# Optimization experiments

Hardware: AMD Instinct MI355X
Metric: run time of the kernel (lower is better)

## Reference

```python
import jax, jax.numpy as jnp
import numpy as np

# Dimensions (Llama-3-8B-style GQA with paged KV cache)
B, S, HID = 1, 1024, 4096
H, HKV, D = 32, 8, 128
G = H // HKV
BLK = 16            # tokens per KV block
NB = 256            # blocks in storage
CB = 192            # context blocks attended (3072 tokens)
PAST = 2048         # tokens already cached before this step
NL = 2              # layers in kv_ptr
L = CB * BLK


def rotate_half(x):
    x1, x2 = x[..., : x.shape[-1] // 2], x[..., x.shape[-1] // 2:]
    return jnp.concatenate([-x2, x1], axis=-1)


def setup_inputs() -> dict:
    key = jax.random.key(0)
    ks = jax.random.split(key, 8)
    hidden_states = jax.random.normal(ks[0], (B, S, HID), jnp.float32)
    kv_ptr = jax.random.normal(ks[1], (NL, 2, NB, HKV, BLK, D), jnp.float32)
    Wq = 0.02 * jax.random.normal(ks[2], (H * D, HID), jnp.float32)
    Wk = 0.02 * jax.random.normal(ks[3], (HKV * D, HID), jnp.float32)
    Wv = 0.02 * jax.random.normal(ks[4], (HKV * D, HID), jnp.float32)
    Wo = 0.02 * jax.random.normal(ks[5], (HID, H * D), jnp.float32)
    # RoPE cache for the new tokens (global positions PAST..PAST+S-1), HF convention
    pos = (PAST + jnp.arange(S)).astype(jnp.float32)
    inv_freq = 1.0 / (10000.0 ** (jnp.arange(0, D, 2, dtype=jnp.float32) / D))
    freqs = pos[:, None] * inv_freq[None, :]                # [S, D/2]
    emb = jnp.concatenate([freqs, freqs], axis=-1)           # [S, D]
    cos = jnp.cos(emb)[None, None]                           # [1,1,S,D]
    sin = jnp.sin(emb)[None, None]
    new_q_lut = jnp.arange(S, dtype=jnp.int32)[None]         # identity query LUT
    new_kv_lut = (CB - S // BLK + jnp.arange(S // BLK, dtype=jnp.int32))[None]  # blocks 128..191
    all_kv_lut = jnp.arange(CB, dtype=jnp.int32)[None]       # blocks 0..191
    kv_pos = jnp.arange(L)
    q_pos = PAST + jnp.arange(S)
    mask = (kv_pos[None, None, :] <= q_pos[None, :, None])   # [1,S,L] causal over global positions
    cmd_groups = jnp.zeros((B, S), jnp.int32)                # split-K scheduling metadata (no math effect)
    return dict(hidden_states=hidden_states, kv_ptr=kv_ptr, new_q_lut=new_q_lut,
                new_kv_lut=new_kv_lut, all_kv_lut=all_kv_lut, mask=mask,
                cmd_groups=cmd_groups, cos=cos, sin=sin, Wq=Wq, Wk=Wk, Wv=Wv, Wo=Wo,
                layer_idx=0)


def reference(hidden_states, kv_ptr, new_q_lut, new_kv_lut, all_kv_lut, mask,
              cmd_groups, cos, sin, Wq, Wk, Wv, Wo, layer_idx):
    b, s, _ = hidden_states.shape
    # QKV projections (no bias)
    q = jnp.einsum('bsh,oh->bso', hidden_states, Wq).reshape(b, s, H, D).transpose(0, 2, 1, 3)
    k = jnp.einsum('bsh,oh->bso', hidden_states, Wk).reshape(b, s, HKV, D).transpose(0, 2, 1, 3)
    v = jnp.einsum('bsh,oh->bso', hidden_states, Wv).reshape(b, s, HKV, D).transpose(0, 2, 1, 3)
    # RoPE
    q = q * cos + rotate_half(q) * sin
    k = k * cos + rotate_half(k) * sin
    # fill_kv_block_storage: scatter new K/V blocks into this layer's storage (b == 1)
    kb = jnp.transpose(k[0].reshape(HKV, s // BLK, BLK, D), (1, 0, 2, 3))  # [nblk,HKV,BLK,D]
    vb = jnp.transpose(v[0].reshape(HKV, s // BLK, BLK, D), (1, 0, 2, 3))
    sk = kv_ptr[layer_idx, 0].at[new_kv_lut[0]].set(kb)
    sv = kv_ptr[layer_idx, 1].at[new_kv_lut[0]].set(vb)
    # qkv_attention: gather context blocks via LUT, masked GQA attention
    ck = jnp.transpose(sk[all_kv_lut[0]], (1, 0, 2, 3)).reshape(HKV, L, D)  # [HKV,L,D]
    cv = jnp.transpose(sv[all_kv_lut[0]], (1, 0, 2, 3)).reshape(HKV, L, D)
    qg = q[:, :, new_q_lut[0], :].reshape(b, HKV, G, s, D)
    scores = jnp.einsum('bkgsd,kld->bkgsl', qg, ck) / jnp.sqrt(jnp.float32(D))
    scores = jnp.where(mask[:, None, None], scores, jnp.finfo(scores.dtype).min)
    p = jax.nn.softmax(scores, axis=-1)
    o = jnp.einsum('bkgsl,kld->bkgsd', p, cv).reshape(b, H, s, D)
    o = o.transpose(0, 2, 1, 3).reshape(b, s, H * D)
    return jnp.einsum('bso,ho->bsh', o, Wo)
```

## Files before the change

kernel.cpp:

```cpp
#include <hip/hip_runtime.h>
#include <cstdint>
#include <cstddef>


typedef _Float16 f16;
typedef f16 f16x8 __attribute__((ext_vector_type(8)));
typedef f16 f16x4 __attribute__((ext_vector_type(4)));
typedef float f32x4 __attribute__((ext_vector_type(4)));

#define HIDN 4096
#define LCTX 3072
#define PASTN 2048
#define QK_SCALE_LOG2 0.12753102734366334f
#define RESC_THR 11.54f

__device__ __forceinline__ f32x4 mfma16(f16x8 a, f16x8 b, f32x4 c) {
    return __builtin_amdgcn_mfma_f32_16x16x32_f16(a, b, c, 0, 0, 0);
}

__device__ __forceinline__ void gl_lds16(const void* g, void* l) {
    auto gp = (const __attribute__((address_space(1))) unsigned int*)(uintptr_t)g;
    auto lp = (__attribute__((address_space(3))) unsigned int*)(uintptr_t)l;
    __builtin_amdgcn_global_load_lds(gp, lp, 16, 0, 0);
}

__device__ __forceinline__ uint32_t lds_lo(const void* p) {
    return (uint32_t)(uintptr_t)p;
}

#define TRRD(dst, va, OFF) \
    asm volatile("ds_read_b64_tr_b16 %0, %1 offset:" #OFF : "=v"(dst) : "v"(va))

__global__ void cvt_f32_f16(const float* __restrict__ src, f16* __restrict__ dst, int n4)
{
    int i = blockIdx.x * 256 + threadIdx.x;
    if (i >= n4) return;
    f32x4 v = *(const f32x4*)(src + (size_t)i * 4);
    f16x4 h;
#pragma unroll
    for (int j = 0; j < 4; j++) h[j] = (f16)v[j];
    *(f16x4*)(dst + (size_t)i * 4) = h;
}

template <int EPI>
__global__ __launch_bounds__(256, 3) void gemm_f16(
    const f16* __restrict__ A, const f16* __restrict__ B,
    float* __restrict__ Cf, f16* __restrict__ Cq, f16* __restrict__ Ck,
    f16* __restrict__ Cv, int M, int N, int K)
{
    __shared__ f16 As[128 * 64];
    __shared__ f16 Bs[128 * 64];

    const int t = threadIdx.x, lane = t & 63, w = t >> 6;
    const int wm = w >> 1, wn = w & 1;
    const int l16 = lane & 15, g16 = lane >> 4;
    const int m0 = blockIdx.y * 128, n0 = blockIdx.x * 128;

    const int srow = lane >> 3;
    const int sgr  = (lane & 7) ^ srow;

    const size_t aoff = (size_t)(m0 + w * 32 + srow) * K + sgr * 8;
    const size_t boff = (size_t)(n0 + w * 32 + srow) * K + sgr * 8;

    f32x4 acc[4][4];
#pragma unroll
    for (int i = 0; i < 4; i++)
#pragma unroll
        for (int j = 0; j < 4; j++) acc[i][j] = (f32x4){0.f, 0.f, 0.f, 0.f};

    for (int k0 = 0; k0 < K; k0 += 64) {
#pragma unroll
        for (int j = 0; j < 4; j++) {
            gl_lds16(A + aoff + (size_t)j * 8 * K + k0, (void*)(As + (w * 32 + j * 8) * 64));
            gl_lds16(B + boff + (size_t)j * 8 * K + k0, (void*)(Bs + (w * 32 + j * 8) * 64));
        }
        __syncthreads();

#pragma unroll
        for (int ks = 0; ks < 2; ks++) {
            f16x8 af[4], bfr[4];
#pragma unroll
            for (int mi = 0; mi < 4; mi++) {
                int r = wm * 64 + mi * 16 + l16;
                int g = ks * 4 + g16;
                af[mi] = *(const f16x8*)&As[r * 64 + ((g ^ (r & 7)) << 3)];
            }
#pragma unroll
            for (int ni = 0; ni < 4; ni++) {
                int r = wn * 64 + ni * 16 + l16;
                int g = ks * 4 + g16;
                bfr[ni] = *(const f16x8*)&Bs[r * 64 + ((g ^ (r & 7)) << 3)];
            }
#pragma unroll
            for (int ni = 0; ni < 4; ni++)
#pragma unroll
                for (int mi = 0; mi < 4; mi++)
                    acc[mi][ni] = mfma16(af[mi], bfr[ni], acc[mi][ni]);
        }
        __syncthreads();
    }

#pragma unroll
    for (int mi = 0; mi < 4; mi++)
#pragma unroll
        for (int ni = 0; ni < 4; ni++)
#pragma unroll
            for (int r = 0; r < 4; r++) {
                int row = m0 + wm * 64 + mi * 16 + (g16 << 2) + r;
                int col = n0 + wn * 64 + ni * 16 + l16;
                float val = acc[mi][ni][r];
                if (EPI == 0) {
                    if (col < 4096) {
                        Cq[(size_t)row * 4096 + col] = (f16)val;
                    } else if (col < 5120) {
                        Ck[(size_t)row * 1024 + (col - 4096)] = (f16)val;
                    } else {
                        int c = col - 5120;
                        int hh = c >> 7, d = c & 127;
                        Cv[((size_t)hh * LCTX + PASTN + row) * 128 + d] = (f16)val;
                    }
                } else {
                    Cf[(size_t)row * N + col] = val;
                }
            }
}

__global__ void rope_q(f16* __restrict__ q, const float* __restrict__ cosp,
                       const float* __restrict__ sinp)
{
    int i = blockIdx.x * 256 + threadIdx.x;
    int gd = i & 7, hh = (i >> 3) & 31, s = i >> 8;
    size_t b1 = (size_t)s * 4096 + hh * 128 + gd * 8;
    f16x8 x1 = *(f16x8*)(q + b1);
    f16x8 x2 = *(f16x8*)(q + b1 + 64);
    const float* c1 = cosp + s * 128 + gd * 8;
    const float* s1 = sinp + s * 128 + gd * 8;
    const float* c2 = c1 + 64;
    const float* s2 = s1 + 64;
    f16x8 o1, o2;
#pragma unroll
    for (int j = 0; j < 8; j++) {
        float a = (float)x1[j], b = (float)x2[j];
        o1[j] = (f16)((a * c1[j] - b * s1[j]) * QK_SCALE_LOG2);
        o2[j] = (f16)((b * c2[j] + a * s2[j]) * QK_SCALE_LOG2);
    }
    *(f16x8*)(q + b1) = o1;
    *(f16x8*)(q + b1 + 64) = o2;
}

__global__ void rope_k(const f16* __restrict__ kraw, const float* __restrict__ cosp,
                       const float* __restrict__ sinp, f16* __restrict__ ck)
{
    int i = blockIdx.x * 256 + threadIdx.x;
    int gd = i & 7, kvh = (i >> 3) & 7, s = i >> 6;
    size_t b1 = (size_t)s * 1024 + kvh * 128 + gd * 8;
    f16x8 x1 = *(const f16x8*)(kraw + b1);
    f16x8 x2 = *(const f16x8*)(kraw + b1 + 64);
    const float* c1 = cosp + s * 128 + gd * 8;
    const float* s1 = sinp + s * 128 + gd * 8;
    const float* c2 = c1 + 64;
    const float* s2 = s1 + 64;
    f16x8 o1, o2;
#pragma unroll
    for (int j = 0; j < 8; j++) {
        float a = (float)x1[j], b = (float)x2[j];
        o1[j] = (f16)(a * c1[j] - b * s1[j]);
        o2[j] = (f16)(b * c2[j] + a * s2[j]);
    }
    size_t dst = ((size_t)kvh * LCTX + PASTN + s) * 128 + gd * 8;
    *(f16x8*)(ck + dst) = o1;
    *(f16x8*)(ck + dst + 64) = o2;
}

__global__ void cache_conv(const float* __restrict__ kvp, const int* __restrict__ layer,
                           f16* __restrict__ ck, f16* __restrict__ cv)
{
    int i4 = blockIdx.x * 256 + threadIdx.x;
    int half = i4 >> 19;
    int e = (i4 & 524287) * 4;
    int hh = e >> 18, rem = e & 262143, l = rem >> 7, d = rem & 127;
    int blk = l >> 4, rr = l & 15;
    size_t src = (((size_t)(layer[0] * 2 + half) * 256 + blk) * 8 + hh) * 2048
               + (size_t)rr * 128 + d;
    f32x4 x = *(const f32x4*)(kvp + src);
    f16x4 h;
#pragma unroll
    for (int j = 0; j < 4; j++) h[j] = (f16)x[j];
    size_t dst = ((size_t)hh * LCTX + l) * 128 + d;
    *(f16x4*)((half ? cv : ck) + dst) = h;
}

__global__ __launch_bounds__(256, 2) void attn_f16(
    const f16* __restrict__ Q, const f16* __restrict__ Kc,
    const f16* __restrict__ Vc, f16* __restrict__ Og)
{
    const int b = blockIdx.x;
    const int idx = b & 255;
    const int h = idx & 31;
    const int jt = idx >> 5;
    const int tile = (b >> 8) ? (15 - jt) : jt;
    const int s0 = tile * 64;
    const int kvh = h >> 2;
    const int t = threadIdx.x, lane = t & 63, w = t >> 6;
    const int l16 = lane & 15, g16 = lane >> 4;

    __shared__ f16 Ks[2][64 * 128];
    __shared__ f16 Vs[2][64 * 128];
    __shared__ f16 Pl[4][16 * 64];

    f16x8 qf[4];
    {
        size_t base = (size_t)(s0 + w * 16 + l16) * 4096 + h * 128;
#pragma unroll
        for (int kk = 0; kk < 4; kk++)
            qf[kk] = *(const f16x8*)(Q + base + kk * 32 + g16 * 8);
    }

    f32x4 of[8];
#pragma unroll
    for (int cf = 0; cf < 8; cf++) of[cf] = (f32x4){0.f, 0.f, 0.f, 0.f};
    float mr = -3.0e38f, lr = 0.f;

    const f16* Kb = Kc + (size_t)kvh * LCTX * 128;
    const f16* Vb = Vc + (size_t)kvh * LCTX * 128;
    const int nt = (PASTN + s0 + 64) >> 6;

    const int krow = lane >> 4;
    const int kp   = lane & 15;
    const int lv = ((lane >> 3) & 3) * 8 + ((lane >> 5) & 1) * 4 + ((lane >> 1) & 3);
    const int vdo = (lane & 1) * 8;

    const uint32_t vs0 = lds_lo(Vs[0]) + lane * 8;
    const uint32_t vs1 = lds_lo(Vs[1]) + lane * 8;

#define STAGE_KV(l0, buf)                                                     \
    {                                                                         \
        _Pragma("unroll")                                                     \
        for (int j = 0; j < 4; j++) {                                         \
            int r7 = ((j & 1) << 2) + krow;                                   \
            int sg = kp ^ r7;                                                 \
            gl_lds16(Kb + (size_t)((l0) + w * 16 + j * 4 + krow) * 128 + sg * 8, \
                     (void*)(Ks[buf] + (w * 16 + j * 4) * 128));              \
        }                                                                     \
        _Pragma("unroll")                                                     \
        for (int q = 0; q < 4; q++) {                                         \
            int idx2 = w * 4 + q;                                             \
            int ks2 = idx2 >> 3, db = idx2 & 7;                               \
            gl_lds16(Vb + (size_t)((l0) + ks2 * 32 + lv) * 128 + db * 16 + vdo, \
                     (void*)(Vs[buf] + ks2 * 4096 + db * 512));               \
        }                                                                     \
    }

    STAGE_KV(0, 0);
    __syncthreads();

    for (int it = 0; it < nt; ++it) {
        const int l0 = it << 6;
        const int cur = it & 1;

        if (it + 1 < nt) STAGE_KV(l0 + 64, cur ^ 1);

        f32x4 sf[4];
#pragma unroll
        for (int ni = 0; ni < 4; ni++) sf[ni] = (f32x4){0.f, 0.f, 0.f, 0.f};
        __builtin_amdgcn_s_setprio(1);
#pragma unroll
        for (int ni = 0; ni < 4; ni++)
#pragma unroll
            for (int kk = 0; kk < 4; kk++) {
                int r = ni * 16 + l16;
                int g = kk * 4 + g16;
                f16x8 kh = *(const f16x8*)&Ks[cur][r * 128 + ((g ^ (r & 7)) << 3)];
                sf[ni] = mfma16(kh, qf[kk], sf[ni]);
            }
        __builtin_amdgcn_s_setprio(0);

        const int qrow = s0 + w * 16 + l16;
        const bool needmask = (l0 + 63 > PASTN + s0);
        if (needmask) {
#pragma unroll
            for (int ni = 0; ni < 4; ni++)
#pragma unroll
                for (int r = 0; r < 4; r++) {
                    int col = l0 + ni * 16 + (g16 << 2) + r;
                    if (col > PASTN + qrow) sf[ni][r] = -3.0e38f;
                }
        }

        float mx;
        {
            f32x4 m4 = sf[0];
#pragma unroll
            for (int ni = 1; ni < 4; ni++) {
                m4[0] = fmaxf(m4[0], sf[ni][0]); m4[1] = fmaxf(m4[1], sf[ni][1]);
                m4[2] = fmaxf(m4[2], sf[ni][2]); m4[3] = fmaxf(m4[3], sf[ni][3]);
            }
            mx = fmaxf(fmaxf(m4[0], m4[1]), fmaxf(m4[2], m4[3]));
        }
        mx = fmaxf(mx, __shfl_xor(mx, 16));
        mx = fmaxf(mx, __shfl_xor(mx, 32));
        if (__any(mx > mr + RESC_THR)) {
            float mnew = fmaxf(mr, mx);
            float corr = exp2f(mr - mnew);
            mr = mnew;
            lr *= corr;
            float cr[4];
#pragma unroll
            for (int r = 0; r < 4; r++) cr[r] = __shfl(corr, (g16 << 2) + r);
#pragma unroll
            for (int cf = 0; cf < 8; cf++)
#pragma unroll
                for (int r = 0; r < 4; r++) of[cf][r] *= cr[r];
        }
        float ss = 0.f;
#pragma unroll
        for (int ni = 0; ni < 4; ni++)
#pragma unroll
            for (int r = 0; r < 4; r++) {
                float p = exp2f(sf[ni][r] - mr);
                sf[ni][r] = p;
                ss += p;
            }
        ss += __shfl_xor(ss, 16);
        ss += __shfl_xor(ss, 32);
        lr += ss;

#pragma unroll
        for (int ni = 0; ni < 4; ni++) {
            f16x4 pv;
#pragma unroll
            for (int r = 0; r < 4; r++) pv[r] = (f16)sf[ni][r];
            int off = l16 * 128 + ((((ni << 1) | (g16 >> 1)) ^ (l16 & 7)) << 4)
                    + ((g16 & 1) << 3);
            *(f16x4*)((char*)&Pl[w][0] + off) = pv;
        }

#pragma unroll
        for (int ks = 0; ks < 2; ks++) {
            int g = ks * 4 + g16;
            f16x8 pa = *(const f16x8*)&Pl[w][l16 * 64 + ((g ^ (l16 & 7)) << 3)];
            uint32_t va = (cur ? vs1 : vs0) + ks * 8192;
            f16x4 t0, t1, t2, t3, t4, t5, t6, t7;
            f16x4 u0, u1, u2, u3, u4, u5, u6, u7;
            TRRD(t0, va, 0);    TRRD(u0, va, 512);
            TRRD(t1, va, 1024); TRRD(u1, va, 1536);
            TRRD(t2, va, 2048); TRRD(u2, va, 2560);
            TRRD(t3, va, 3072); TRRD(u3, va, 3584);
            TRRD(t4, va, 4096); TRRD(u4, va, 4608);
            TRRD(t5, va, 5120); TRRD(u5, va, 5632);
            TRRD(t6, va, 6144); TRRD(u6, va, 6656);
            TRRD(t7, va, 7168); TRRD(u7, va, 7680);
            asm volatile("s_waitcnt lgkmcnt(0)" ::: "memory");
            __builtin_amdgcn_sched_barrier(0);
            __builtin_amdgcn_s_setprio(1);
#define PV_MFMA(cf, lo, hi)                                        \
            {                                                      \
                f16x8 vb;                                          \
                vb[0] = lo[0]; vb[1] = lo[1]; vb[2] = lo[2];       \
                vb[3] = lo[3]; vb[4] = hi[0]; vb[5] = hi[1];       \
                vb[6] = hi[2]; vb[7] = hi[3];                      \
                of[cf] = mfma16(pa, vb, of[cf]);                   \
            }
            PV_MFMA(0, t0, u0) PV_MFMA(1, t1, u1)
            PV_MFMA(2, t2, u2) PV_MFMA(3, t3, u3)
            PV_MFMA(4, t4, u4) PV_MFMA(5, t5, u5)
            PV_MFMA(6, t6, u6) PV_MFMA(7, t7, u7)
#undef PV_MFMA
            __builtin_amdgcn_s_setprio(0);
        }
        __syncthreads();
    }

    float lrr[4];
#pragma unroll
    for (int r = 0; r < 4; r++) lrr[r] = __shfl(lr, (g16 << 2) + r);
#pragma unroll
    for (int cf = 0; cf < 8; cf++)
#pragma unroll
        for (int r = 0; r < 4; r++) {
            int srow = s0 + w * 16 + (g16 << 2) + r;
            int d = cf * 16 + l16;
            Og[(size_t)srow * 4096 + (size_t)h * 128 + d] = (f16)(of[cf][r] / lrr[r]);
        }
#undef STAGE_KV
}

extern "C" void kernel_launch(void* const* d_in, const int* in_sizes, int n_in,
                              void* d_out, int out_size, void* d_ws, size_t ws_size,
                              hipStream_t stream)
{
    const float* hidden = (const float*)d_in[0];
    const float* kvp    = (const float*)d_in[1];
    const float* cosp   = (const float*)d_in[7];
    const float* sinp   = (const float*)d_in[8];
    const float* Wq     = (const float*)d_in[9];
    const float* Wk     = (const float*)d_in[10];
    const float* Wv     = (const float*)d_in[11];
    const float* Wo     = (const float*)d_in[12];
    const int*   layer  = (const int*)d_in[13];

    char* ws = (char*)d_ws;
    f16* w16  = (f16*)ws;
    f16* h16  = (f16*)(ws + 50331648);
    f16* ck   = (f16*)(ws + 58720256);
    f16* cv   = (f16*)(ws + 65011712);
    f16* obuf = (f16*)(ws + 71303168);

    f16* q16  = (f16*)d_out;
    f16* kraw = (f16*)((char*)d_out + 8388608);

    cvt_f32_f16<<<4096,  256, 0, stream>>>(hidden, h16, 1048576);
    cvt_f32_f16<<<16384, 256, 0, stream>>>(Wq, w16, 4194304);
    cvt_f32_f16<<<4096,  256, 0, stream>>>(Wk, w16 + (size_t)4096 * 4096, 1048576);
    cvt_f32_f16<<<4096,  256, 0, stream>>>(Wv, w16 + (size_t)5120 * 4096, 1048576);

    gemm_f16<0><<<dim3(48, 8), 256, 0, stream>>>(
        h16, w16, nullptr, q16, kraw, cv, 1024, 6144, 4096);

    cvt_f32_f16<<<16384, 256, 0, stream>>>(Wo, w16, 4194304);

    rope_q<<<1024, 256, 0, stream>>>(q16, cosp, sinp);
    rope_k<<<256, 256, 0, stream>>>(kraw, cosp, sinp, ck);
    cache_conv<<<4096, 256, 0, stream>>>(kvp, layer, ck, cv);

    attn_f16<<<dim3(512), 256, 0, stream>>>(q16, ck, cv, obuf);

    gemm_f16<1><<<dim3(32, 8), 256, 0, stream>>>(
        obuf, w16, (float*)d_out, nullptr, nullptr, nullptr, 1024, 4096, 4096);
}
```

Baseline: 287.8 us.

## Keep P in registers for PV via 16x16x16 MFMA, merge conversion kernels

The attention kernel no longer writes the softmax probabilities to LDS and reads them back. It feeds the per-lane P fragments straight into 16x16x16 MFMAs and relays out the V staging to match. The V transpose-reads are interleaved with the MFMAs using partial lgkmcnt waits, and the row-sum reduction moves out of the loop to the end. Separately, four f32-to-f16 conversion launches are merged into one kernel to cut launch overhead. The trade-off is twice as many smaller MFMAs and more live registers.

```diff
diff --git a/kernel.cpp b/kernel.cpp
--- a/kernel.cpp
+++ b/kernel.cpp
@@ -17,6 +17,9 @@
 __device__ __forceinline__ f32x4 mfma16(f16x8 a, f16x8 b, f32x4 c) {
     return __builtin_amdgcn_mfma_f32_16x16x32_f16(a, b, c, 0, 0, 0);
 }
+__device__ __forceinline__ f32x4 mfma16k16(f16x4 a, f16x4 b, f32x4 c) {
+    return __builtin_amdgcn_mfma_f32_16x16x16f16(a, b, c, 0, 0, 0);
+}
 
 __device__ __forceinline__ void gl_lds16(const void* g, void* l) {
     auto gp = (const __attribute__((address_space(1))) unsigned int*)(uintptr_t)g;
@@ -30,6 +33,26 @@
 
 #define TRRD(dst, va, OFF) \
     asm volatile("ds_read_b64_tr_b16 %0, %1 offset:" #OFF : "=v"(dst) : "v"(va))
+#define WAITL(N) \
+    asm volatile("s_waitcnt lgkmcnt(" #N ")" ::: "memory"); \
+    __builtin_amdgcn_sched_barrier(0)
+
+__global__ void cvt_all(const float* __restrict__ hidden, const float* __restrict__ Wq,
+                        const float* __restrict__ Wk, const float* __restrict__ Wv,
+                        f16* __restrict__ h16, f16* __restrict__ w16)
+{
+    int i = blockIdx.x * 256 + threadIdx.x;
+    const float* src; f16* dst; int off;
+    if (i < 1048576)      { src = hidden; dst = h16; off = i; }
+    else if (i < 5242880) { src = Wq; dst = w16; off = i - 1048576; }
+    else if (i < 6291456) { src = Wk; dst = w16 + (size_t)4096 * 4096; off = i - 5242880; }
+    else                  { src = Wv; dst = w16 + (size_t)5120 * 4096; off = i - 6291456; }
+    f32x4 v = *(const f32x4*)(src + (size_t)off * 4);
+    f16x4 h;
+#pragma unroll
+    for (int j = 0; j < 4; j++) h[j] = (f16)v[j];
+    *(f16x4*)(dst + (size_t)off * 4) = h;
+}
 
 __global__ void cvt_f32_f16(const float* __restrict__ src, f16* __restrict__ dst, int n4)
 {
@@ -206,7 +229,6 @@
 
     __shared__ f16 Ks[2][64 * 128];
     __shared__ f16 Vs[2][64 * 128];
-    __shared__ f16 Pl[4][16 * 64];
 
     f16x8 qf[4];
     {
@@ -227,8 +249,8 @@
 
     const int krow = lane >> 4;
     const int kp   = lane & 15;
-    const int lv = ((lane >> 3) & 3) * 8 + ((lane >> 5) & 1) * 4 + ((lane >> 1) & 3);
-    const int vdo = (lane & 1) * 8;
+    const int vrow = ((lane >> 5) << 4) + (((lane >> 3) & 3) << 2) + ((lane >> 1) & 3);
+    const int vch  = (lane & 1) << 3;
 
     const uint32_t vs0 = lds_lo(Vs[0]) + lane * 8;
     const uint32_t vs1 = lds_lo(Vs[1]) + lane * 8;
@@ -244,10 +266,9 @@
         }                                                                     \
         _Pragma("unroll")                                                     \
         for (int q = 0; q < 4; q++) {                                         \
-            int idx2 = w * 4 + q;                                             \
-            int ks2 = idx2 >> 3, db = idx2 & 7;                               \
-            gl_lds16(Vb + (size_t)((l0) + ks2 * 32 + lv) * 128 + db * 16 + vdo, \
-                     (void*)(Vs[buf] + ks2 * 4096 + db * 512));               \
+            gl_lds16(Vb + (size_t)((l0) + (q & 1) * 32 + vrow) * 128          \
+                        + (w * 2 + (q >> 1)) * 16 + vch,                      \
+                     (void*)(Vs[buf] + (w * 4 + q) * 512));                   \
         }                                                                     \
     }
 
@@ -312,65 +333,60 @@
 #pragma unroll
                 for (int r = 0; r < 4; r++) of[cf][r] *= cr[r];
         }
-        float ss = 0.f;
 #pragma unroll
         for (int ni = 0; ni < 4; ni++)
 #pragma unroll
             for (int r = 0; r < 4; r++) {
                 float p = exp2f(sf[ni][r] - mr);
                 sf[ni][r] = p;
-                ss += p;
-            }
-        ss += __shfl_xor(ss, 16);
-        ss += __shfl_xor(ss, 32);
-        lr += ss;
-
+                lr += p;
+            }
+
+        f16x4 pa[4];
 #pragma unroll
         for (int ni = 0; ni < 4; ni++) {
-            f16x4 pv;
-#pragma unroll
-            for (int r = 0; r < 4; r++) pv[r] = (f16)sf[ni][r];
-            int off = l16 * 128 + ((((ni << 1) | (g16 >> 1)) ^ (l16 & 7)) << 4)
-                    + ((g16 & 1) << 3);
-            *(f16x4*)((char*)&Pl[w][0] + off) = pv;
-        }
-
-#pragma unroll
-        for (int ks = 0; ks < 2; ks++) {
-            int g = ks * 4 + g16;
-            f16x8 pa = *(const f16x8*)&Pl[w][l16 * 64 + ((g ^ (l16 & 7)) << 3)];
-            uint32_t va = (cur ? vs1 : vs0) + ks * 8192;
-            f16x4 t0, t1, t2, t3, t4, t5, t6, t7;
-            f16x4 u0, u1, u2, u3, u4, u5, u6, u7;
-            TRRD(t0, va, 0);    TRRD(u0, va, 512);
-            TRRD(t1, va, 1024); TRRD(u1, va, 1536);
-            TRRD(t2, va, 2048); TRRD(u2, va, 2560);
-            TRRD(t3, va, 3072); TRRD(u3, va, 3584);
-            TRRD(t4, va, 4096); TRRD(u4, va, 4608);
-            TRRD(t5, va, 5120); TRRD(u5, va, 5632);
-            TRRD(t6, va, 6144); TRRD(u6, va, 6656);
-            TRRD(t7, va, 7168); TRRD(u7, va, 7680);
-            asm volatile("s_waitcnt lgkmcnt(0)" ::: "memory");
-            __builtin_amdgcn_sched_barrier(0);
+            pa[ni][0] = (f16)sf[ni][0]; pa[ni][1] = (f16)sf[ni][1];
+            pa[ni][2] = (f16)sf[ni][2]; pa[ni][3] = (f16)sf[ni][3];
+        }
+
+        {
+            const uint32_t va = cur ? vs1 : vs0;
+            f16x4 r0,r1,r2,r3,r4,r5,r6,r7,r8,r9,r10,r11,r12,r13,r14,r15,
+                  r16,r17,r18,r19,r20,r21,r22,r23,r24,r25,r26,r27,r28,r29,r30,r31;
             __builtin_amdgcn_s_setprio(1);
-#define PV_MFMA(cf, lo, hi)                                        \
-            {                                                      \
-                f16x8 vb;                                          \
-                vb[0] = lo[0]; vb[1] = lo[1]; vb[2] = lo[2];       \
-                vb[3] = lo[3]; vb[4] = hi[0]; vb[5] = hi[1];       \
-                vb[6] = hi[2]; vb[7] = hi[3];                      \
-                of[cf] = mfma16(pa, vb, of[cf]);                   \
-            }
-            PV_MFMA(0, t0, u0) PV_MFMA(1, t1, u1)
-            PV_MFMA(2, t2, u2) PV_MFMA(3, t3, u3)
-            PV_MFMA(4, t4, u4) PV_MFMA(5, t5, u5)
-            PV_MFMA(6, t6, u6) PV_MFMA(7, t7, u7)
-#undef PV_MFMA
+            TRRD(r0,va,0);      TRRD(r1,va,512);    TRRD(r2,va,1024);   TRRD(r3,va,1536);
+            TRRD(r4,va,2048);   TRRD(r5,va,2560);   TRRD(r6,va,3072);   TRRD(r7,va,3584);
+            TRRD(r8,va,4096);   TRRD(r9,va,4608);   TRRD(r10,va,5120);  TRRD(r11,va,5632);
+#define X16(cf, ni, reg) of[cf] = mfma16k16(pa[ni], reg, of[cf]);
+            WAITL(8);
+            X16(0,0,r0)  X16(0,1,r1)  X16(0,2,r2)  X16(0,3,r3)
+            TRRD(r12,va,6144);  TRRD(r13,va,6656);  TRRD(r14,va,7168);  TRRD(r15,va,7680);
+            WAITL(8);
+            X16(1,0,r4)  X16(1,1,r5)  X16(1,2,r6)  X16(1,3,r7)
+            TRRD(r16,va,8192);  TRRD(r17,va,8704);  TRRD(r18,va,9216);  TRRD(r19,va,9728);
+            WAITL(8);
+            X16(2,0,r8)  X16(2,1,r9)  X16(2,2,r10) X16(2,3,r11)
+            TRRD(r20,va,10240); TRRD(r21,va,10752); TRRD(r22,va,11264); TRRD(r23,va,11776);
+            WAITL(8);
+            X16(3,0,r12) X16(3,1,r13) X16(3,2,r14) X16(3,3,r15)
+            TRRD(r24,va,12288); TRRD(r25,va,12800); TRRD(r26,va,13312); TRRD(r27,va,13824);
+            WAITL(8);
+            X16(4,0,r16) X16(4,1,r17) X16(4,2,r18) X16(4,3,r19)
+            TRRD(r28,va,14336); TRRD(r29,va,14848); TRRD(r30,va,15360); TRRD(r31,va,15872);
+            WAITL(8);
+            X16(5,0,r20) X16(5,1,r21) X16(5,2,r22) X16(5,3,r23)
+            WAITL(4);
+            X16(6,0,r24) X16(6,1,r25) X16(6,2,r26) X16(6,3,r27)
+            WAITL(0);
+            X16(7,0,r28) X16(7,1,r29) X16(7,2,r30) X16(7,3,r31)
+#undef X16
             __builtin_amdgcn_s_setprio(0);
         }
         __syncthreads();
     }
 
+    lr += __shfl_xor(lr, 16);
+    lr += __shfl_xor(lr, 32);
     float lrr[4];
 #pragma unroll
     for (int r = 0; r < 4; r++) lrr[r] = __shfl(lr, (g16 << 2) + r);
@@ -409,10 +425,7 @@
     f16* q16  = (f16*)d_out;
     f16* kraw = (f16*)((char*)d_out + 8388608);
 
-    cvt_f32_f16<<<4096,  256, 0, stream>>>(hidden, h16, 1048576);
-    cvt_f32_f16<<<16384, 256, 0, stream>>>(Wq, w16, 4194304);
-    cvt_f32_f16<<<4096,  256, 0, stream>>>(Wk, w16 + (size_t)4096 * 4096, 1048576);
-    cvt_f32_f16<<<4096,  256, 0, stream>>>(Wv, w16 + (size_t)5120 * 4096, 1048576);
+    cvt_all<<<28672, 256, 0, stream>>>(hidden, Wq, Wk, Wv, h16, w16);
 
     gemm_f16<0><<<dim3(48, 8), 256, 0, stream>>>(
         h16, w16, nullptr, q16, kraw, cv, 1024, 6144, 4096);
```

Measured after the change: 277.6 us. 3.6% less time.
